# Kernel tuning notes

Hardware: AMD Instinct MI355X
Metric: run time of the kernel (lower is better)

The kernel has to match this reference:

```python
import jax, jax.numpy as jnp
import numpy as np

HEADS = 8
DIM_HEAD = 64
SCALE = DIM_HEAD ** -0.5


def setup_inputs() -> dict:
    key = jax.random.key(0)
    ks = jax.random.split(key, 7)
    b, n, m = 2, 4096, 4096
    query_dim, context_dim, inner = 1024, 768, HEADS * DIM_HEAD
    s = 0.02
    return {
        "x": jax.random.normal(ks[0], (b, n, query_dim), jnp.float32),
        "context": jax.random.normal(ks[1], (b, m, context_dim), jnp.float32),
        "Wq": jax.random.normal(ks[2], (query_dim, inner), jnp.float32) * s,
        "Wk": jax.random.normal(ks[3], (context_dim, inner), jnp.float32) * s,
        "Wv": jax.random.normal(ks[4], (context_dim, inner), jnp.float32) * s,
        "Wo": jax.random.normal(ks[5], (inner, query_dim), jnp.float32) * s,
        "bo": jnp.zeros((query_dim,), jnp.float32),
    }


def reference(x, context, Wq, Wk, Wv, Wo, bo):
    b, n, _ = x.shape
    m = context.shape[1]
    # projections (no bias), split heads: b n (h d) -> b n h d
    q = (x @ Wq).reshape(b, n, HEADS, DIM_HEAD)
    k = (context @ Wk).reshape(b, m, HEADS, DIM_HEAD)
    v = (context @ Wv).reshape(b, m, HEADS, DIM_HEAD)
    # fp32 QK^T (ATTN_PRECISION='fp32' path), full [b,h,n,m] scores
    sim = jnp.einsum("bihd,bjhd->bhij", q.astype(jnp.float32), k.astype(jnp.float32)) * SCALE
    attn = jax.nn.softmax(sim, axis=-1).astype(v.dtype)
    out = jnp.einsum("bhij,bjhd->bihd", attn, v).reshape(b, n, HEADS * DIM_HEAD)
    # to_out: Linear with bias (dropout=0 is identity)
    return out @ Wo + bo
```

## Files before the change

### kernel.cpp

```cpp
#include <hip/hip_runtime.h>
#include <hip/hip_bf16.h>
#include <cmath>


using bf16_t = __hip_bfloat16;
typedef __bf16 bf16x8 __attribute__((ext_vector_type(8)));
typedef float  f32x4  __attribute__((ext_vector_type(4)));

static constexpr int BATCH = 2;
static constexpr int NQ    = 4096;
static constexpr int NKV   = 4096;
static constexpr int NH    = 8;
static constexpr int DH    = 64;
static constexpr int INNER = NH * DH;
static constexpr int QDIM  = 1024;
static constexpr int CDIM  = 768;
static constexpr float QSCALE = 0.125f * 1.4426950408889634f;

#define MFMA_BF16(a, b, c) __builtin_amdgcn_mfma_f32_16x16x32_bf16((a), (b), (c), 0, 0, 0)

__device__ __forceinline__ float fast_exp2(float x) {
  return __builtin_amdgcn_exp2f(x);
}

__device__ __forceinline__ void gload16(const bf16_t* g, bf16_t* l) {
  __builtin_amdgcn_global_load_lds((__attribute__((address_space(1))) void*)(g),
                                   (__attribute__((address_space(3))) void*)(l),
                                   16, 0, 0);
}

__global__ __launch_bounds__(256) void cast2_kernel(const float* __restrict__ x,
                                                    bf16_t* __restrict__ xb, int xn8,
                                                    const float* __restrict__ c,
                                                    bf16_t* __restrict__ cb, int cn8) {
  int id = blockIdx.x * 256 + threadIdx.x;
  const float* in;
  bf16_t* out;
  if (id < xn8) {
    in = x; out = xb;
  } else {
    id -= xn8;
    if (id >= cn8) return;
    in = c; out = cb;
  }
  float4 a = ((const float4*)in)[2 * id];
  float4 b = ((const float4*)in)[2 * id + 1];
  bf16_t t[8] = {__float2bfloat16(a.x), __float2bfloat16(a.y), __float2bfloat16(a.z),
                 __float2bfloat16(a.w), __float2bfloat16(b.x), __float2bfloat16(b.y),
                 __float2bfloat16(b.z), __float2bfloat16(b.w)};
  ((uint4*)out)[id] = *(const uint4*)t;
}

__global__ __launch_bounds__(256) void wtrans4_kernel(const float* __restrict__ Wq,
                                                      const float* __restrict__ Wk,
                                                      const float* __restrict__ Wv,
                                                      const float* __restrict__ Wo,
                                                      bf16_t* __restrict__ WqT,
                                                      bf16_t* __restrict__ WkvT,
                                                      bf16_t* __restrict__ WoT) {
  __shared__ float tile[32][33];
  const float* W;
  bf16_t* WT;
  int K, N;
  switch (blockIdx.z) {
    case 0: W = Wq; WT = WqT; K = QDIM; N = INNER; break;
    case 1: W = Wk; WT = WkvT; K = CDIM; N = INNER; break;
    case 2: W = Wv; WT = WkvT + (size_t)INNER * CDIM; K = CDIM; N = INNER; break;
    default: W = Wo; WT = WoT; K = INNER; N = QDIM; break;
  }
  const int bn = blockIdx.x * 32, bk = blockIdx.y * 32;
  if (bn >= N || bk >= K) return;
  const int tx = threadIdx.x & 31, ty = threadIdx.x >> 5;
  for (int yy = ty; yy < 32; yy += 8)
    tile[yy][tx] = W[(size_t)(bk + yy) * N + bn + tx];
  __syncthreads();
  for (int yy = ty; yy < 32; yy += 8)
    WT[(size_t)(bn + yy) * K + bk + tx] = __float2bfloat16(tile[tx][yy]);
}

__device__ __forceinline__ void gemm64_core(const bf16_t* __restrict__ A,
                                            const bf16_t* __restrict__ WT, int K,
                                            int m0, int n0, int tid,
                                            f32x4 (&acc)[2][4],
                                            bf16_t (*As)[64][32],
                                            bf16_t (*Bs)[128][32]) {
  const int lane = tid & 63, wave = tid >> 6;
  const int lane15 = lane & 15, quad = lane >> 4;
  const int wm = (wave >> 1) * 32, wn = (wave & 1) * 64;
  const int srow = tid >> 2, sc8 = (tid & 3) * 8;
  const bf16_t* aptr = A + (size_t)(m0 + srow) * K + sc8;
  const bf16_t* bptr = WT + (size_t)(n0 + srow) * K + sc8;
  bf16_t* const abase = &As[0][wave * 16][0];
  bf16_t* const bbase = &Bs[0][wave * 16][0];
  constexpr int ABUF = 64 * 32, BBUF = 128 * 32;

  auto stage = [&](int t, int cur) {
    const bf16_t* as = aptr + t * 32;
    const bf16_t* bs = bptr + t * 32;
    gload16(as, abase + cur * ABUF);
    gload16(bs, bbase + cur * BBUF);
    gload16(bs + (size_t)64 * K, bbase + cur * BBUF + 64 * 32);
  };

  const int T = K / 32;
  stage(0, 0);
  for (int t = 0; t < T; ++t) {
    const int cur = t & 1;
    __syncthreads();
    if (t + 1 < T) stage(t + 1, cur ^ 1);
    bf16x8 af[2], bfr[4];
    for (int i = 0; i < 2; ++i)
      af[i] = *reinterpret_cast<const bf16x8*>(&As[cur][wm + i * 16 + lane15][quad * 8]);
    for (int j = 0; j < 4; ++j)
      bfr[j] = *reinterpret_cast<const bf16x8*>(&Bs[cur][wn + j * 16 + lane15][quad * 8]);
    for (int i = 0; i < 2; ++i)
      for (int j = 0; j < 4; ++j) acc[i][j] = MFMA_BF16(af[i], bfr[j], acc[i][j]);
  }
}

__global__ __launch_bounds__(256) void qkv_gemm_kernel(const bf16_t* __restrict__ xb,
                                                       const bf16_t* __restrict__ ctxb,
                                                       const bf16_t* __restrict__ WqT,
                                                       const bf16_t* __restrict__ WkvT,
                                                       bf16_t* __restrict__ qob,
                                                       bf16_t* __restrict__ kb,
                                                       bf16_t* __restrict__ vtb) {
  __shared__ __align__(16) bf16_t As[2][64][32];
  __shared__ __align__(16) bf16_t Bs[2][128][32];
  const int tid = threadIdx.x;
  const bool isq = blockIdx.y < 4;
  const bf16_t* A  = isq ? xb : ctxb;
  const bf16_t* WT = isq ? WqT : WkvT;
  const int K  = isq ? QDIM : CDIM;
  const int m0 = blockIdx.x * 64;
  const int n0 = (isq ? blockIdx.y : blockIdx.y - 4) * 128;

  const f32x4 vzero = {0.f, 0.f, 0.f, 0.f};
  f32x4 acc[2][4];
  for (int i = 0; i < 2; ++i)
    for (int j = 0; j < 4; ++j) acc[i][j] = vzero;

  gemm64_core(A, WT, K, m0, n0, tid, acc, As, Bs);

  const int lane = tid & 63, wave = tid >> 6;
  const int lane15 = lane & 15, quad = lane >> 4;
  const int wm = (wave >> 1) * 32, wn = (wave & 1) * 64;
  for (int i = 0; i < 2; ++i) {
    int gm = m0 + wm + i * 16 + quad * 4;
    for (int j = 0; j < 4; ++j) {
      int gn = n0 + wn + j * 16 + lane15;
      for (int r = 0; r < 4; ++r) {
        float v = acc[i][j][r];
        if (isq) {
          qob[(size_t)(gm + r) * INNER + gn] = __float2bfloat16(v * QSCALE);
        } else if (gn < INNER) {
          kb[(size_t)(gm + r) * INNER + gn] = __float2bfloat16(v);
        } else {
          int gmr = gm + r;
          vtb[((size_t)(gmr >> 12) * INNER + (gn - INNER)) * (size_t)NKV +
              (gmr & 4095)] = __float2bfloat16(v);
        }
      }
    }
  }
}

__global__ __launch_bounds__(256) void out_gemm_kernel(const bf16_t* __restrict__ A,
                                                       const bf16_t* __restrict__ WT,
                                                       float* __restrict__ C,
                                                       const float* __restrict__ bias) {
  __shared__ __align__(16) bf16_t As[2][64][32];
  __shared__ __align__(16) bf16_t Bs[2][128][32];
  const int tid = threadIdx.x;
  const int m0 = blockIdx.x * 64, n0 = blockIdx.y * 128;
  constexpr int K = INNER, N = QDIM;

  const f32x4 vzero = {0.f, 0.f, 0.f, 0.f};
  f32x4 acc[2][4];
  for (int i = 0; i < 2; ++i)
    for (int j = 0; j < 4; ++j) acc[i][j] = vzero;

  gemm64_core(A, WT, K, m0, n0, tid, acc, As, Bs);

  const int lane = tid & 63, wave = tid >> 6;
  const int lane15 = lane & 15, quad = lane >> 4;
  const int wm = (wave >> 1) * 32, wn = (wave & 1) * 64;
  for (int i = 0; i < 2; ++i) {
    int gm = m0 + wm + i * 16 + quad * 4;
    for (int j = 0; j < 4; ++j) {
      int gn = n0 + wn + j * 16 + lane15;
      for (int r = 0; r < 4; ++r)
        C[(size_t)(gm + r) * N + gn] = acc[i][j][r] + bias[gn];
    }
  }
}

__global__ __launch_bounds__(512) void attn_kernel(const bf16_t* Qg ,
                                                   const bf16_t* __restrict__ Kg ,
                                                   const bf16_t* __restrict__ Vtg ,
                                                   bf16_t* Og ) {
  __shared__ __align__(16) bf16_t KsF[2][8][512];
  __shared__ __align__(16) bf16_t VtF[2][8][512];
  __shared__ __align__(16) bf16_t PsA[128][72];

  const int tid = threadIdx.x;
  const int lane = tid & 63, wave = tid >> 6;
  const int lane15 = lane & 15, quad = lane >> 4;
  const int wrow = wave * 16;
  const int q0 = blockIdx.x * 128;
  const int h = blockIdx.y;
  const int b = blockIdx.z;

  const size_t qbase  = ((size_t)b * NQ + q0) * INNER + h * DH;
  const size_t kbase  = ((size_t)b * NKV) * INNER + h * DH;
  const size_t vtbase = ((size_t)(b * NH + h) * DH) * NKV;

  bf16x8 qf[2];
  for (int ks = 0; ks < 2; ++ks)
    qf[ks] = *reinterpret_cast<const bf16x8*>(
        Qg + qbase + (size_t)(wrow + lane15) * INNER + ks * 32 + quad * 8);

  bf16x8 ones;
  for (int i = 0; i < 8; ++i) ones[i] = (__bf16)1.0f;

  const f32x4 vzero = {0.f, 0.f, 0.f, 0.f};
  f32x4 acc_o[4];
  f32x4 acc_l = vzero;
  for (int j = 0; j < 4; ++j) acc_o[j] = vzero;

  const int cw = wave;
  auto kaddr = [&](int kv0) {
    return Kg + kbase + (size_t)(kv0 + (cw & 3) * 16 + lane15) * INNER + (cw >> 2) * 32 + quad * 8;
  };
  auto vaddr = [&](int kv0) {
    return Vtg + vtbase + (size_t)((cw & 3) * 16 + lane15) * NKV + kv0 + (cw >> 2) * 32 + quad * 8;
  };
  uint4 kr = *(const uint4*)kaddr(0);
  uint4 vr = *(const uint4*)vaddr(0);

  constexpr int T = NKV / 64;
  for (int t = 0; t < T; ++t) {
    const int cur = t & 1;
    *(uint4*)&KsF[cur][cw][lane * 8] = kr;
    *(uint4*)&VtF[cur][cw][lane * 8] = vr;
    __syncthreads();

    f32x4 acc_st[4];
    for (int j = 0; j < 4; ++j) acc_st[j] = vzero;
    __builtin_amdgcn_s_setprio(1);
    for (int ks = 0; ks < 2; ++ks) {
      bf16x8 kf[4];
      for (int j = 0; j < 4; ++j)
        kf[j] = *reinterpret_cast<const bf16x8*>(&KsF[cur][ks * 4 + j][lane * 8]);
      for (int j = 0; j < 4; ++j) acc_st[j] = MFMA_BF16(kf[j], qf[ks], acc_st[j]);
    }
    __builtin_amdgcn_s_setprio(0);

    if (t + 1 < T) {
      int kv0n = (t + 1) * 64;
      kr = *(const uint4*)kaddr(kv0n);
      vr = *(const uint4*)vaddr(kv0n);
    }

    for (int j = 0; j < 4; ++j) {
      bf16_t t4[4];
      for (int r = 0; r < 4; ++r)
        t4[r] = __float2bfloat16(fast_exp2(acc_st[j][r]));
      *(uint2*)&PsA[wrow + lane15][j * 16 + quad * 4] = *(const uint2*)t4;
    }
    asm volatile("s_waitcnt lgkmcnt(0)" ::: "memory");

    __builtin_amdgcn_s_setprio(1);
    for (int ks = 0; ks < 2; ++ks) {
      bf16x8 pf, vf[4];
      pf = *reinterpret_cast<const bf16x8*>(&PsA[wrow + lane15][ks * 32 + quad * 8]);
      for (int j = 0; j < 4; ++j)
        vf[j] = *reinterpret_cast<const bf16x8*>(&VtF[cur][ks * 4 + j][lane * 8]);
      acc_l = MFMA_BF16(pf, ones, acc_l);
      for (int j = 0; j < 4; ++j) acc_o[j] = MFMA_BF16(pf, vf[j], acc_o[j]);
    }
    __builtin_amdgcn_s_setprio(0);
  }

  for (int r = 0; r < 4; ++r) {
    float invr = 1.f / acc_l[r];
    int row = wrow + quad * 4 + r;
    for (int j = 0; j < 4; ++j)
      Og[qbase + (size_t)row * INNER + j * 16 + lane15] =
          __float2bfloat16(acc_o[j][r] * invr);
  }
}

extern "C" void kernel_launch(void* const* d_in, const int* in_sizes, int n_in,
                              void* d_out, int out_size, void* d_ws, size_t ws_size,
                              hipStream_t stream) {
  (void)in_sizes; (void)n_in; (void)out_size; (void)ws_size;
  const float* x   = (const float*)d_in[0];
  const float* ctx = (const float*)d_in[1];
  const float* Wq  = (const float*)d_in[2];
  const float* Wk  = (const float*)d_in[3];
  const float* Wv  = (const float*)d_in[4];
  const float* Wo  = (const float*)d_in[5];
  const float* bo  = (const float*)d_in[6];
  float* out = (float*)d_out;

  char* ws = (char*)d_ws;
  size_t off = 0;
  auto take = [&](size_t nelem) { bf16_t* p = (bf16_t*)(ws + off); off += nelem * 2; return p; };
  bf16_t* WqT  = take((size_t)INNER * QDIM);
  bf16_t* WkvT = take((size_t)(2 * INNER) * CDIM);
  bf16_t* WoT  = take((size_t)QDIM * INNER);
  bf16_t* qob  = take((size_t)BATCH * NQ * INNER);
  bf16_t* kb   = take((size_t)BATCH * NKV * INNER);
  bf16_t* vtb  = take((size_t)BATCH * INNER * NKV);

  bf16_t* xb   = (bf16_t*)d_out;
  bf16_t* ctxb = xb + (size_t)BATCH * NQ * QDIM;

  const int M = BATCH * NQ;
  const int xN8 = BATCH * NQ * QDIM / 8, cN8 = BATCH * NKV * CDIM / 8;

  cast2_kernel<<<(xN8 + cN8 + 255) / 256, 256, 0, stream>>>(x, xb, xN8, ctx, ctxb, cN8);
  wtrans4_kernel<<<dim3(32, 32, 4), 256, 0, stream>>>(Wq, Wk, Wv, Wo, WqT, WkvT, WoT);

  qkv_gemm_kernel<<<dim3(M / 64, 12), 256, 0, stream>>>(xb, ctxb, WqT, WkvT, qob, kb, vtb);

  attn_kernel<<<dim3(NQ / 128, NH, BATCH), 512, 0, stream>>>(qob, kb, vtb, qob);

  out_gemm_kernel<<<dim3(M / 64, QDIM / 128), 256, 0, stream>>>(qob, WoT, out, bo);
}
```

Measured before the change: 262.7 us.

## Enlarge GEMM tiles with triple-buffered swizzled LDS and halve attention block waves

The projection GEMMs move from 64x128 to 128x128 tiles with a three-stage LDS ring, an XOR swizzle on the LDS layout, and explicit vmcnt waits in place of __syncthreads. The attention kernel drops to 256 threads, with each wave handling 32 query rows and staging two K/V chunks. It also issues the next tile's global loads before the QK MMAs. These changes aim to raise operand reuse per LDS load, hide global latency and cut bank conflicts. The cost is more registers and LDS per block, which may reduce occupancy.

Measured after the change: 240.0 us. 1.09x faster.

```diff
diff --git a/kernel.cpp b/kernel.cpp
--- a/kernel.cpp
+++ b/kernel.cpp
@@ -78,74 +78,93 @@
     WT[(size_t)(bn + yy) * K + bk + tx] = __float2bfloat16(tile[tx][yy]);
 }
 
-__device__ __forceinline__ void gemm64_core(const bf16_t* __restrict__ A,
-                                            const bf16_t* __restrict__ WT, int K,
-                                            int m0, int n0, int tid,
-                                            f32x4 (&acc)[2][4],
-                                            bf16_t (*As)[64][32],
-                                            bf16_t (*Bs)[128][32]) {
+__device__ __forceinline__ void gemm128_core(const bf16_t* __restrict__ A,
+                                             const bf16_t* __restrict__ WT, int K,
+                                             int m0, int n0, int tid,
+                                             f32x4 (&acc)[4][4],
+                                             bf16_t (*As)[128][32],
+                                             bf16_t (*Bs)[128][32]) {
   const int lane = tid & 63, wave = tid >> 6;
   const int lane15 = lane & 15, quad = lane >> 4;
-  const int wm = (wave >> 1) * 32, wn = (wave & 1) * 64;
-  const int srow = tid >> 2, sc8 = (tid & 3) * 8;
-  const bf16_t* aptr = A + (size_t)(m0 + srow) * K + sc8;
-  const bf16_t* bptr = WT + (size_t)(n0 + srow) * K + sc8;
-  bf16_t* const abase = &As[0][wave * 16][0];
-  bf16_t* const bbase = &Bs[0][wave * 16][0];
-  constexpr int ABUF = 64 * 32, BBUF = 128 * 32;
-
-  auto stage = [&](int t, int cur) {
+  const int wm = (wave >> 1) * 64, wn = (wave & 1) * 64;
+  const int srow = tid >> 2;
+  const int scol = ((tid & 3) ^ ((srow >> 1) & 3)) * 8;
+  const bf16_t* aptr = A + (size_t)(m0 + srow) * K + scol;
+  const bf16_t* bptr = WT + (size_t)(n0 + srow) * K + scol;
+  bf16_t* const ab = &As[0][wave * 16][0];
+  bf16_t* const bb = &Bs[0][wave * 16][0];
+  constexpr int BUF = 128 * 32;
+
+  auto stage = [&](int t) {
+    const int c = (t % 3) * BUF;
     const bf16_t* as = aptr + t * 32;
     const bf16_t* bs = bptr + t * 32;
-    gload16(as, abase + cur * ABUF);
-    gload16(bs, bbase + cur * BBUF);
-    gload16(bs + (size_t)64 * K, bbase + cur * BBUF + 64 * 32);
+    gload16(as, ab + c);
+    gload16(as + (size_t)64 * K, ab + c + 64 * 32);
+    gload16(bs, bb + c);
+    gload16(bs + (size_t)64 * K, bb + c + 64 * 32);
   };
 
   const int T = K / 32;
-  stage(0, 0);
+  stage(0);
+  stage(1);
   for (int t = 0; t < T; ++t) {
-    const int cur = t & 1;
-    __syncthreads();
-    if (t + 1 < T) stage(t + 1, cur ^ 1);
-    bf16x8 af[2], bfr[4];
-    for (int i = 0; i < 2; ++i)
-      af[i] = *reinterpret_cast<const bf16x8*>(&As[cur][wm + i * 16 + lane15][quad * 8]);
-    for (int j = 0; j < 4; ++j)
-      bfr[j] = *reinterpret_cast<const bf16x8*>(&Bs[cur][wn + j * 16 + lane15][quad * 8]);
-    for (int i = 0; i < 2; ++i)
+    const int cur = t % 3;
+    if (t < T - 1) {
+      asm volatile("s_waitcnt vmcnt(4)" ::: "memory");
+    } else {
+      asm volatile("s_waitcnt vmcnt(0)" ::: "memory");
+    }
+    asm volatile("s_barrier" ::: "memory");
+    if (t + 2 < T) stage(t + 2);
+    bf16x8 af[4], bfr[4];
+#pragma unroll
+    for (int i = 0; i < 4; ++i) {
+      const int row = wm + i * 16 + lane15;
+      af[i] = *reinterpret_cast<const bf16x8*>(
+          &As[cur][0][0] + row * 32 + ((quad * 8) ^ (((row >> 1) & 3) * 8)));
+    }
+#pragma unroll
+    for (int j = 0; j < 4; ++j) {
+      const int row = wn + j * 16 + lane15;
+      bfr[j] = *reinterpret_cast<const bf16x8*>(
+          &Bs[cur][0][0] + row * 32 + ((quad * 8) ^ (((row >> 1) & 3) * 8)));
+    }
+#pragma unroll
+    for (int i = 0; i < 4; ++i)
+#pragma unroll
       for (int j = 0; j < 4; ++j) acc[i][j] = MFMA_BF16(af[i], bfr[j], acc[i][j]);
   }
 }
 
-__global__ __launch_bounds__(256) void qkv_gemm_kernel(const bf16_t* __restrict__ xb,
-                                                       const bf16_t* __restrict__ ctxb,
-                                                       const bf16_t* __restrict__ WqT,
-                                                       const bf16_t* __restrict__ WkvT,
-                                                       bf16_t* __restrict__ qob,
-                                                       bf16_t* __restrict__ kb,
-                                                       bf16_t* __restrict__ vtb) {
-  __shared__ __align__(16) bf16_t As[2][64][32];
-  __shared__ __align__(16) bf16_t Bs[2][128][32];
+__global__ __launch_bounds__(256, 3) void qkv_gemm_kernel(const bf16_t* __restrict__ xb,
+                                                          const bf16_t* __restrict__ ctxb,
+                                                          const bf16_t* __restrict__ WqT,
+                                                          const bf16_t* __restrict__ WkvT,
+                                                          bf16_t* __restrict__ qob,
+                                                          bf16_t* __restrict__ kb,
+                                                          bf16_t* __restrict__ vtb) {
+  __shared__ __align__(16) bf16_t As[3][128][32];
+  __shared__ __align__(16) bf16_t Bs[3][128][32];
   const int tid = threadIdx.x;
   const bool isq = blockIdx.y < 4;
   const bf16_t* A  = isq ? xb : ctxb;
   const bf16_t* WT = isq ? WqT : WkvT;
   const int K  = isq ? QDIM : CDIM;
-  const int m0 = blockIdx.x * 64;
+  const int m0 = blockIdx.x * 128;
   const int n0 = (isq ? blockIdx.y : blockIdx.y - 4) * 128;
 
   const f32x4 vzero = {0.f, 0.f, 0.f, 0.f};
-  f32x4 acc[2][4];
-  for (int i = 0; i < 2; ++i)
+  f32x4 acc[4][4];
+  for (int i = 0; i < 4; ++i)
     for (int j = 0; j < 4; ++j) acc[i][j] = vzero;
 
-  gemm64_core(A, WT, K, m0, n0, tid, acc, As, Bs);
+  gemm128_core(A, WT, K, m0, n0, tid, acc, As, Bs);
 
   const int lane = tid & 63, wave = tid >> 6;
   const int lane15 = lane & 15, quad = lane >> 4;
-  const int wm = (wave >> 1) * 32, wn = (wave & 1) * 64;
-  for (int i = 0; i < 2; ++i) {
+  const int wm = (wave >> 1) * 64, wn = (wave & 1) * 64;
+  for (int i = 0; i < 4; ++i) {
     int gm = m0 + wm + i * 16 + quad * 4;
     for (int j = 0; j < 4; ++j) {
       int gn = n0 + wn + j * 16 + lane15;
@@ -165,40 +184,42 @@
   }
 }
 
-__global__ __launch_bounds__(256) void out_gemm_kernel(const bf16_t* __restrict__ A,
-                                                       const bf16_t* __restrict__ WT,
-                                                       float* __restrict__ C,
-                                                       const float* __restrict__ bias) {
-  __shared__ __align__(16) bf16_t As[2][64][32];
-  __shared__ __align__(16) bf16_t Bs[2][128][32];
+__global__ __launch_bounds__(256, 3) void out_gemm_kernel(const bf16_t* __restrict__ A,
+                                                          const bf16_t* __restrict__ WT,
+                                                          float* __restrict__ C,
+                                                          const float* __restrict__ bias) {
+  __shared__ __align__(16) bf16_t As[3][128][32];
+  __shared__ __align__(16) bf16_t Bs[3][128][32];
   const int tid = threadIdx.x;
-  const int m0 = blockIdx.x * 64, n0 = blockIdx.y * 128;
+  const int m0 = blockIdx.x * 128, n0 = blockIdx.y * 128;
   constexpr int K = INNER, N = QDIM;
 
   const f32x4 vzero = {0.f, 0.f, 0.f, 0.f};
-  f32x4 acc[2][4];
-  for (int i = 0; i < 2; ++i)
+  f32x4 acc[4][4];
+  for (int i = 0; i < 4; ++i)
     for (int j = 0; j < 4; ++j) acc[i][j] = vzero;
 
-  gemm64_core(A, WT, K, m0, n0, tid, acc, As, Bs);
+  gemm128_core(A, WT, K, m0, n0, tid, acc, As, Bs);
 
   const int lane = tid & 63, wave = tid >> 6;
   const int lane15 = lane & 15, quad = lane >> 4;
-  const int wm = (wave >> 1) * 32, wn = (wave & 1) * 64;
-  for (int i = 0; i < 2; ++i) {
+  const int wm = (wave >> 1) * 64, wn = (wave & 1) * 64;
+  float bv[4];
+  for (int j = 0; j < 4; ++j) bv[j] = bias[n0 + wn + j * 16 + lane15];
+  for (int i = 0; i < 4; ++i) {
     int gm = m0 + wm + i * 16 + quad * 4;
     for (int j = 0; j < 4; ++j) {
       int gn = n0 + wn + j * 16 + lane15;
       for (int r = 0; r < 4; ++r)
-        C[(size_t)(gm + r) * N + gn] = acc[i][j][r] + bias[gn];
-    }
-  }
-}
-
-__global__ __launch_bounds__(512) void attn_kernel(const bf16_t* Qg ,
-                                                   const bf16_t* __restrict__ Kg ,
-                                                   const bf16_t* __restrict__ Vtg ,
-                                                   bf16_t* Og ) {
+        C[(size_t)(gm + r) * N + gn] = acc[i][j][r] + bv[j];
+    }
+  }
+}
+
+__global__ __launch_bounds__(256, 2) void attn_kernel(const bf16_t* Qg ,
+                                                      const bf16_t* __restrict__ Kg ,
+                                                      const bf16_t* __restrict__ Vtg ,
+                                                      bf16_t* Og ) {
   __shared__ __align__(16) bf16_t KsF[2][8][512];
   __shared__ __align__(16) bf16_t VtF[2][8][512];
   __shared__ __align__(16) bf16_t PsA[128][72];
@@ -206,7 +227,7 @@
   const int tid = threadIdx.x;
   const int lane = tid & 63, wave = tid >> 6;
   const int lane15 = lane & 15, quad = lane >> 4;
-  const int wrow = wave * 16;
+  const int wrow = wave * 32;
   const int q0 = blockIdx.x * 128;
   const int h = blockIdx.y;
   const int b = blockIdx.z;
@@ -215,80 +236,107 @@
   const size_t kbase  = ((size_t)b * NKV) * INNER + h * DH;
   const size_t vtbase = ((size_t)(b * NH + h) * DH) * NKV;
 
-  bf16x8 qf[2];
+  bf16x8 qf[2][2];
   for (int ks = 0; ks < 2; ++ks)
-    qf[ks] = *reinterpret_cast<const bf16x8*>(
-        Qg + qbase + (size_t)(wrow + lane15) * INNER + ks * 32 + quad * 8);
+    for (int qh = 0; qh < 2; ++qh)
+      qf[ks][qh] = *reinterpret_cast<const bf16x8*>(
+          Qg + qbase + (size_t)(wrow + qh * 16 + lane15) * INNER + ks * 32 + quad * 8);
 
   bf16x8 ones;
   for (int i = 0; i < 8; ++i) ones[i] = (__bf16)1.0f;
 
   const f32x4 vzero = {0.f, 0.f, 0.f, 0.f};
-  f32x4 acc_o[4];
-  f32x4 acc_l = vzero;
-  for (int j = 0; j < 4; ++j) acc_o[j] = vzero;
-
-  const int cw = wave;
-  auto kaddr = [&](int kv0) {
-    return Kg + kbase + (size_t)(kv0 + (cw & 3) * 16 + lane15) * INNER + (cw >> 2) * 32 + quad * 8;
+  f32x4 acc_o[2][4];
+  f32x4 acc_l[2];
+  for (int qh = 0; qh < 2; ++qh) {
+    acc_l[qh] = vzero;
+    for (int j = 0; j < 4; ++j) acc_o[qh][j] = vzero;
+  }
+
+  const int c0 = wave * 2, c1 = wave * 2 + 1;
+  auto kaddr = [&](int c, int kv0) {
+    return Kg + kbase + (size_t)(kv0 + (c & 3) * 16 + lane15) * INNER + (c >> 2) * 32 + quad * 8;
   };
-  auto vaddr = [&](int kv0) {
-    return Vtg + vtbase + (size_t)((cw & 3) * 16 + lane15) * NKV + kv0 + (cw >> 2) * 32 + quad * 8;
+  auto vaddr = [&](int c, int kv0) {
+    return Vtg + vtbase + (size_t)((c & 3) * 16 + lane15) * NKV + kv0 + (c >> 2) * 32 + quad * 8;
   };
-  uint4 kr = *(const uint4*)kaddr(0);
-  uint4 vr = *(const uint4*)vaddr(0);
+  uint4 kr0 = *(const uint4*)kaddr(c0, 0), kr1 = *(const uint4*)kaddr(c1, 0);
+  uint4 vr0 = *(const uint4*)vaddr(c0, 0), vr1 = *(const uint4*)vaddr(c1, 0);
 
   constexpr int T = NKV / 64;
   for (int t = 0; t < T; ++t) {
     const int cur = t & 1;
-    *(uint4*)&KsF[cur][cw][lane * 8] = kr;
-    *(uint4*)&VtF[cur][cw][lane * 8] = vr;
+    *(uint4*)&KsF[cur][c0][lane * 8] = kr0;
+    *(uint4*)&KsF[cur][c1][lane * 8] = kr1;
+    *(uint4*)&VtF[cur][c0][lane * 8] = vr0;
+    *(uint4*)&VtF[cur][c1][lane * 8] = vr1;
     __syncthreads();
 
-    f32x4 acc_st[4];
-    for (int j = 0; j < 4; ++j) acc_st[j] = vzero;
+    if (t + 1 < T) {
+      const int kv0n = (t + 1) * 64;
+      kr0 = *(const uint4*)kaddr(c0, kv0n);
+      kr1 = *(const uint4*)kaddr(c1, kv0n);
+      vr0 = *(const uint4*)vaddr(c0, kv0n);
+      vr1 = *(const uint4*)vaddr(c1, kv0n);
+    }
+
+    f32x4 acc_st[2][4];
+#pragma unroll
+    for (int qh = 0; qh < 2; ++qh)
+      for (int j = 0; j < 4; ++j) acc_st[qh][j] = vzero;
     __builtin_amdgcn_s_setprio(1);
+#pragma unroll
     for (int ks = 0; ks < 2; ++ks) {
       bf16x8 kf[4];
+#pragma unroll
       for (int j = 0; j < 4; ++j)
         kf[j] = *reinterpret_cast<const bf16x8*>(&KsF[cur][ks * 4 + j][lane * 8]);
-      for (int j = 0; j < 4; ++j) acc_st[j] = MFMA_BF16(kf[j], qf[ks], acc_st[j]);
+#pragma unroll
+      for (int qh = 0; qh < 2; ++qh)
+#pragma unroll
+        for (int j = 0; j < 4; ++j)
+          acc_st[qh][j] = MFMA_BF16(kf[j], qf[ks][qh], acc_st[qh][j]);
     }
     __builtin_amdgcn_s_setprio(0);
 
-    if (t + 1 < T) {
-      int kv0n = (t + 1) * 64;
-      kr = *(const uint4*)kaddr(kv0n);
-      vr = *(const uint4*)vaddr(kv0n);
-    }
-
-    for (int j = 0; j < 4; ++j) {
-      bf16_t t4[4];
-      for (int r = 0; r < 4; ++r)
-        t4[r] = __float2bfloat16(fast_exp2(acc_st[j][r]));
-      *(uint2*)&PsA[wrow + lane15][j * 16 + quad * 4] = *(const uint2*)t4;
-    }
+#pragma unroll
+    for (int qh = 0; qh < 2; ++qh)
+#pragma unroll
+      for (int j = 0; j < 4; ++j) {
+        bf16_t t4[4];
+        for (int r = 0; r < 4; ++r)
+          t4[r] = __float2bfloat16(fast_exp2(acc_st[qh][j][r]));
+        *(uint2*)&PsA[wrow + qh * 16 + lane15][j * 16 + quad * 4] = *(const uint2*)t4;
+      }
     asm volatile("s_waitcnt lgkmcnt(0)" ::: "memory");
 
     __builtin_amdgcn_s_setprio(1);
+#pragma unroll
     for (int ks = 0; ks < 2; ++ks) {
-      bf16x8 pf, vf[4];
-      pf = *reinterpret_cast<const bf16x8*>(&PsA[wrow + lane15][ks * 32 + quad * 8]);
+      bf16x8 vf[4];
+#pragma unroll
       for (int j = 0; j < 4; ++j)
         vf[j] = *reinterpret_cast<const bf16x8*>(&VtF[cur][ks * 4 + j][lane * 8]);
-      acc_l = MFMA_BF16(pf, ones, acc_l);
-      for (int j = 0; j < 4; ++j) acc_o[j] = MFMA_BF16(pf, vf[j], acc_o[j]);
+#pragma unroll
+      for (int qh = 0; qh < 2; ++qh) {
+        bf16x8 pf = *reinterpret_cast<const bf16x8*>(
+            &PsA[wrow + qh * 16 + lane15][ks * 32 + quad * 8]);
+        acc_l[qh] = MFMA_BF16(pf, ones, acc_l[qh]);
+#pragma unroll
+        for (int j = 0; j < 4; ++j) acc_o[qh][j] = MFMA_BF16(pf, vf[j], acc_o[qh][j]);
+      }
     }
     __builtin_amdgcn_s_setprio(0);
   }
 
-  for (int r = 0; r < 4; ++r) {
-    float invr = 1.f / acc_l[r];
-    int row = wrow + quad * 4 + r;
-    for (int j = 0; j < 4; ++j)
-      Og[qbase + (size_t)row * INNER + j * 16 + lane15] =
-          __float2bfloat16(acc_o[j][r] * invr);
-  }
+  for (int qh = 0; qh < 2; ++qh)
+    for (int r = 0; r < 4; ++r) {
+      float invr = 1.f / acc_l[qh][r];
+      int row = wrow + qh * 16 + quad * 4 + r;
+      for (int j = 0; j < 4; ++j)
+        Og[qbase + (size_t)row * INNER + j * 16 + lane15] =
+            __float2bfloat16(acc_o[qh][j][r] * invr);
+    }
 }
 
 extern "C" void kernel_launch(void* const* d_in, const int* in_sizes, int n_in,
@@ -323,9 +371,9 @@
   cast2_kernel<<<(xN8 + cN8 + 255) / 256, 256, 0, stream>>>(x, xb, xN8, ctx, ctxb, cN8);
   wtrans4_kernel<<<dim3(32, 32, 4), 256, 0, stream>>>(Wq, Wk, Wv, Wo, WqT, WkvT, WoT);
 
-  qkv_gemm_kernel<<<dim3(M / 64, 12), 256, 0, stream>>>(xb, ctxb, WqT, WkvT, qob, kb, vtb);
-
-  attn_kernel<<<dim3(NQ / 128, NH, BATCH), 512, 0, stream>>>(qob, kb, vtb, qob);
-
-  out_gemm_kernel<<<dim3(M / 64, QDIM / 128), 256, 0, stream>>>(qob, WoT, out, bo);
-}
+  qkv_gemm_kernel<<<dim3(M / 128, 12), 256, 0, stream>>>(xb, ctxb, WqT, WkvT, qob, kb, vtb);
+
+  attn_kernel<<<dim3(NQ / 128, NH, BATCH), 256, 0, stream>>>(qob, kb, vtb, qob);
+
+  out_gemm_kernel<<<dim3(M / 128, QDIM / 128), 256, 0, stream>>>(qob, WoT, out, bo);
+}
```
